# Performance work log

Measured on AMD Instinct MI355X. Metric: run time of the kernel, lower is better.

## Reference

```python
import jax, jax.numpy as jnp
import numpy as np


def setup_inputs() -> dict:
    key = jax.random.key(0)
    k1, k2, k3 = jax.random.split(key, 3)
    N, K, d, d_out = 100000, 32, 64, 64
    x = jax.random.normal(k1, (N, d), dtype=jnp.float32)
    edge_index = jax.random.randint(k2, (N, K), 0, N, dtype=jnp.int64)
    W = jax.random.normal(k3, (2 * d, d_out), dtype=jnp.float32) * (1.0 / np.sqrt(2 * d))
    b = jnp.zeros((d_out,), dtype=jnp.float32)
    return {"x": x, "edge_index": edge_index, "W": W, "b": b}


def reference(x, edge_index, W, b):
    # x: [N, d], edge_index: [N, K] dense neighbor indices
    x_j = x[edge_index]                                  # [N, K, d] gather
    # concat([x_i, x_j - x_i]) then max over K. The x_i half is constant over K,
    # so its max is x itself; max of the diff half computed directly (same math,
    # avoids materializing the [N, K, 2d] concat).
    diff_max = jnp.max(x_j - x[:, None, :], axis=1)      # [N, d]
    h = jnp.concatenate([x, diff_max], axis=-1)          # [N, 2d]
    return h @ W + b                                     # [N, d_out]
```

## Files before the change

### kernel.cpp

```cpp
#include <hip/hip_runtime.h>
#include <hip/hip_bf16.h>
#include <cstdint>


typedef __attribute__((ext_vector_type(8))) short short8;
typedef __attribute__((ext_vector_type(4))) float f4;

#define TILE 16
#define ROWS 168

__device__ __forceinline__ unsigned short f2bf(float f) {
  unsigned int u = __builtin_bit_cast(unsigned int, f);
  u += 0x7fffu + ((u >> 16) & 1u);
  return (unsigned short)(u >> 16);
}
__device__ __forceinline__ unsigned int pack2(float a, float b) {
  return (unsigned int)f2bf(a) | ((unsigned int)f2bf(b) << 16);
}
__device__ __forceinline__ float bflo(unsigned int u) {
  return __builtin_bit_cast(float, u << 16);
}
__device__ __forceinline__ float bfhi(unsigned int u) {
  return __builtin_bit_cast(float, u & 0xffff0000u);
}

__global__ __launch_bounds__(256)
void convert_kernel(const float* __restrict__ x, unsigned int* __restrict__ xbf, int n8) {
  int i = blockIdx.x * 256 + threadIdx.x;
  if (i >= n8) return;
  const f4* p = (const f4*)x + (size_t)i * 2;
  f4 a = p[0], b = p[1];
  uint4 w;
  w.x = pack2(a.x, a.y); w.y = pack2(a.z, a.w);
  w.z = pack2(b.x, b.y); w.w = pack2(b.z, b.w);
  ((uint4*)xbf)[i] = w;
}

__global__ __launch_bounds__(256, 6)
void mrconv2_kernel(const unsigned int* __restrict__ xbf,
                    const int* __restrict__ ei,
                    const float* __restrict__ W,
                    const float* __restrict__ bias,
                    float* __restrict__ out,
                    int n_tiles)
{
  __shared__ __align__(16) unsigned short hs[TILE * ROWS];
  __shared__ __align__(16) int eis[TILE * 32];
  __shared__ __align__(16) float otile[TILE * 64];

  const int tid  = threadIdx.x;
  const int wv   = tid >> 6;
  const int lane = tid & 63;
  const int c = lane & 15;
  const int g = lane >> 4;
  const int t2 = lane >> 5;
  const int h  = (lane >> 3) & 3;
  const int e  = lane & 7;

  const int node0 = blockIdx.x * TILE;

  short8 bfrag[4];
  #pragma unroll
  for (int ks = 0; ks < 4; ++ks) {
    short8 v;
    #pragma unroll
    for (int j = 0; j < 8; ++j)
      v[j] = (short)f2bf(W[(ks * 32 + g * 8 + j) * 64 + wv * 16 + c]);
    bfrag[ks] = v;
  }

  *(int2*)&eis[tid * 2] = *(const int2*)(ei + (size_t)node0 * 32 + tid * 2);
  __syncthreads();

  const float NEG = -3.4e38f;
  #pragma unroll
  for (int tt = 0; tt < 2; ++tt) {
    const int t = wv * 4 + tt * 2 + t2;
    const uint4 xr = *(const uint4*)(xbf + (size_t)(node0 + t) * 32 + e * 4);
    const float xi0 = bflo(xr.x), xi1 = bfhi(xr.x);
    const float xi2 = bflo(xr.y), xi3 = bfhi(xr.y);
    const float xi4 = bflo(xr.z), xi5 = bfhi(xr.z);
    const float xi6 = bflo(xr.w), xi7 = bfhi(xr.w);
    float m0 = NEG, m1 = NEG, m2 = NEG, m3 = NEG;
    float m4 = NEG, m5 = NEG, m6 = NEG, m7 = NEG;
    #pragma unroll
    for (int it = 0; it < 8; ++it) {
      const int j = eis[t * 32 + it * 4 + h];
      const uint4 r = *(const uint4*)(xbf + (size_t)j * 32 + e * 4);
      m0 = fmaxf(m0, bflo(r.x) - xi0);
      m1 = fmaxf(m1, bfhi(r.x) - xi1);
      m2 = fmaxf(m2, bflo(r.y) - xi2);
      m3 = fmaxf(m3, bfhi(r.y) - xi3);
      m4 = fmaxf(m4, bflo(r.z) - xi4);
      m5 = fmaxf(m5, bfhi(r.z) - xi5);
      m6 = fmaxf(m6, bflo(r.w) - xi6);
      m7 = fmaxf(m7, bfhi(r.w) - xi7);
    }
    m0 = fmaxf(m0, __shfl_xor(m0, 8));  m1 = fmaxf(m1, __shfl_xor(m1, 8));
    m2 = fmaxf(m2, __shfl_xor(m2, 8));  m3 = fmaxf(m3, __shfl_xor(m3, 8));
    m4 = fmaxf(m4, __shfl_xor(m4, 8));  m5 = fmaxf(m5, __shfl_xor(m5, 8));
    m6 = fmaxf(m6, __shfl_xor(m6, 8));  m7 = fmaxf(m7, __shfl_xor(m7, 8));
    m0 = fmaxf(m0, __shfl_xor(m0, 16)); m1 = fmaxf(m1, __shfl_xor(m1, 16));
    m2 = fmaxf(m2, __shfl_xor(m2, 16)); m3 = fmaxf(m3, __shfl_xor(m3, 16));
    m4 = fmaxf(m4, __shfl_xor(m4, 16)); m5 = fmaxf(m5, __shfl_xor(m5, 16));
    m6 = fmaxf(m6, __shfl_xor(m6, 16)); m7 = fmaxf(m7, __shfl_xor(m7, 16));

    if (h == 1) {
      *(uint4*)(hs + t * ROWS + e * 8) = xr;
    } else if (h == 0) {
      uint4 w;
      w.x = pack2(m0, m1); w.y = pack2(m2, m3);
      w.z = pack2(m4, m5); w.w = pack2(m6, m7);
      *(uint4*)(hs + t * ROWS + 64 + e * 8) = w;
    }
  }
  __syncthreads();

  f4 acc = {0.f, 0.f, 0.f, 0.f};
  #pragma unroll
  for (int ks = 0; ks < 4; ++ks) {
    short8 a = *(const short8*)(hs + c * ROWS + ks * 32 + g * 8);
    acc = __builtin_amdgcn_mfma_f32_16x16x32_bf16(a, bfrag[ks], acc, 0, 0, 0);
  }

  const float bb = bias[wv * 16 + c];
  #pragma unroll
  for (int j = 0; j < 4; ++j)
    otile[(g * 4 + j) * 64 + wv * 16 + c] = acc[j] + bb;
  __syncthreads();
  *(f4*)(out + (size_t)node0 * 64 + tid * 4) = *(const f4*)&otile[tid * 4];
}

#define FWPB 4
#define FROWS 160
__global__ __launch_bounds__(256, 4)
void mrconv_fp32_kernel(const float* __restrict__ x,
                        const int* __restrict__ ei,
                        const float* __restrict__ W,
                        const float* __restrict__ bias,
                        float* __restrict__ out,
                        int n_tiles)
{
  __shared__ __align__(16) unsigned short hsf[FWPB][TILE * FROWS];
  const int wave = threadIdx.x >> 6;
  const int lane = threadIdx.x & 63;
  const int c = lane & 15;
  const int g = lane >> 4;

  short8 bfrag[4][4];
  #pragma unroll
  for (int ks = 0; ks < 4; ++ks) {
    #pragma unroll
    for (int nt = 0; nt < 4; ++nt) {
      short8 v;
      #pragma unroll
      for (int j = 0; j < 8; ++j) {
        int k = ks * 32 + g * 8 + j;
        v[j] = (short)f2bf(W[k * 64 + nt * 16 + c]);
      }
      bfrag[ks][nt] = v;
    }
  }

  const int tile = blockIdx.x * FWPB + wave;
  if (tile >= n_tiles) return;
  const int node0 = tile * TILE;
  unsigned short* hrow = &hsf[wave][0];

  #pragma unroll 2
  for (int t = 0; t < TILE; ++t) {
    const int n = node0 + t;
    const f4 xi = *(const f4*)(x + (size_t)n * 64 + 4 * c);
    f4 m = { -3.4e38f, -3.4e38f, -3.4e38f, -3.4e38f };
    #pragma unroll
    for (int it = 0; it < 8; ++it) {
      const int j = ei[(size_t)n * 32 + it * 4 + g];
      const f4 xj = *(const f4*)(x + (size_t)j * 64 + 4 * c);
      m.x = fmaxf(m.x, xj.x - xi.x);
      m.y = fmaxf(m.y, xj.y - xi.y);
      m.z = fmaxf(m.z, xj.z - xi.z);
      m.w = fmaxf(m.w, xj.w - xi.w);
    }
    m.x = fmaxf(m.x, __shfl_xor(m.x, 16));
    m.y = fmaxf(m.y, __shfl_xor(m.y, 16));
    m.z = fmaxf(m.z, __shfl_xor(m.z, 16));
    m.w = fmaxf(m.w, __shfl_xor(m.w, 16));
    m.x = fmaxf(m.x, __shfl_xor(m.x, 32));
    m.y = fmaxf(m.y, __shfl_xor(m.y, 32));
    m.z = fmaxf(m.z, __shfl_xor(m.z, 32));
    m.w = fmaxf(m.w, __shfl_xor(m.w, 32));
    if (g == 0) {
      ushort4 p;
      p.x = f2bf(xi.x); p.y = f2bf(xi.y); p.z = f2bf(xi.z); p.w = f2bf(xi.w);
      *(ushort4*)(hrow + t * FROWS + 4 * c) = p;
    } else if (g == 1) {
      ushort4 p;
      p.x = f2bf(m.x); p.y = f2bf(m.y); p.z = f2bf(m.z); p.w = f2bf(m.w);
      *(ushort4*)(hrow + t * FROWS + 64 + 4 * c) = p;
    }
  }
  __asm__ volatile("s_waitcnt lgkmcnt(0)" ::: "memory");

  f4 acc[4] = {{0.f,0.f,0.f,0.f},{0.f,0.f,0.f,0.f},{0.f,0.f,0.f,0.f},{0.f,0.f,0.f,0.f}};
  #pragma unroll
  for (int ks = 0; ks < 4; ++ks) {
    short8 a = *(const short8*)(hrow + c * FROWS + ks * 32 + g * 8);
    #pragma unroll
    for (int nt = 0; nt < 4; ++nt)
      acc[nt] = __builtin_amdgcn_mfma_f32_16x16x32_bf16(a, bfrag[ks][nt], acc[nt], 0, 0, 0);
  }
  const int rbase = node0 + g * 4;
  #pragma unroll
  for (int nt = 0; nt < 4; ++nt) {
    const float bb = bias[nt * 16 + c];
    #pragma unroll
    for (int j = 0; j < 4; ++j)
      out[(size_t)(rbase + j) * 64 + nt * 16 + c] = acc[nt][j] + bb;
  }
}

extern "C" void kernel_launch(void* const* d_in, const int* in_sizes, int n_in,
                              void* d_out, int out_size, void* d_ws, size_t ws_size,
                              hipStream_t stream) {
  const float* x  = (const float*)d_in[0];
  const int*   ei = (const int*)d_in[1];
  const float* W  = (const float*)d_in[2];
  const float* b  = (const float*)d_in[3];
  float* out = (float*)d_out;

  const int N = in_sizes[0] / 64;
  const int n_tiles = N / TILE;

  const size_t need = (size_t)N * 64 * 2;
  if (ws_size >= need) {
    unsigned int* xbf = (unsigned int*)d_ws;
    const int n8 = N * 64 / 8;
    hipLaunchKernelGGL(convert_kernel, dim3((n8 + 255) / 256), dim3(256), 0, stream,
                       x, xbf, n8);
    hipLaunchKernelGGL(mrconv2_kernel, dim3(n_tiles), dim3(256), 0, stream,
                       xbf, ei, W, b, out, n_tiles);
  } else {
    const int blocks = (n_tiles + FWPB - 1) / FWPB;
    hipLaunchKernelGGL(mrconv_fp32_kernel, dim3(blocks), dim3(256), 0, stream,
                       x, ei, W, b, out, n_tiles);
  }
}
```

Before: 135.7 us.

## Prepack bf16 W fragments once, hoist x_i subtraction out of neighbor max

New measurement: 130.6 us. 1.04x faster.

```diff
diff --git a/kernel.cpp b/kernel.cpp
--- a/kernel.cpp
+++ b/kernel.cpp
@@ -25,21 +25,37 @@
 }
 
 __global__ __launch_bounds__(256)
-void convert_kernel(const float* __restrict__ x, unsigned int* __restrict__ xbf, int n8) {
-  int i = blockIdx.x * 256 + threadIdx.x;
-  if (i >= n8) return;
-  const f4* p = (const f4*)x + (size_t)i * 2;
-  f4 a = p[0], b = p[1];
-  uint4 w;
-  w.x = pack2(a.x, a.y); w.y = pack2(a.z, a.w);
-  w.z = pack2(b.x, b.y); w.w = pack2(b.z, b.w);
-  ((uint4*)xbf)[i] = w;
+void convert_kernel(const float* __restrict__ x, unsigned int* __restrict__ xbf,
+                    const float* __restrict__ W, unsigned short* __restrict__ wf,
+                    int n8, int nxb) {
+  if ((int)blockIdx.x < nxb) {
+    int i = blockIdx.x * 256 + threadIdx.x;
+    if (i >= n8) return;
+    const f4* p = (const f4*)x + (size_t)i * 2;
+    f4 a = p[0], b = p[1];
+    uint4 w;
+    w.x = pack2(a.x, a.y); w.y = pack2(a.z, a.w);
+    w.z = pack2(b.x, b.y); w.w = pack2(b.z, b.w);
+    ((uint4*)xbf)[i] = w;
+  } else {
+    #pragma unroll
+    for (int q = 0; q < 4; ++q) {
+      int idx = threadIdx.x * 4 + q;
+      int wv = idx >> 8, ks = (idx >> 6) & 3, l = idx & 63;
+      int c = l & 15, g = l >> 4;
+      short8 v;
+      #pragma unroll
+      for (int j = 0; j < 8; ++j)
+        v[j] = (short)f2bf(W[(ks * 32 + g * 8 + j) * 64 + wv * 16 + c]);
+      *(short8*)(wf + (size_t)idx * 8) = v;
+    }
+  }
 }
 
 __global__ __launch_bounds__(256, 6)
-void mrconv2_kernel(const unsigned int* __restrict__ xbf,
+void mrconv3_kernel(const unsigned int* __restrict__ xbf,
+                    const unsigned short* __restrict__ wf,
                     const int* __restrict__ ei,
-                    const float* __restrict__ W,
                     const float* __restrict__ bias,
                     float* __restrict__ out,
                     int n_tiles)
@@ -53,66 +69,54 @@
   const int lane = tid & 63;
   const int c = lane & 15;
   const int g = lane >> 4;
-  const int t2 = lane >> 5;
-  const int h  = (lane >> 3) & 3;
+  const int t2 = lane >> 4;
+  const int h  = (lane >> 3) & 1;
   const int e  = lane & 7;
 
   const int node0 = blockIdx.x * TILE;
+  const int t = wv * 4 + t2;
 
   short8 bfrag[4];
   #pragma unroll
-  for (int ks = 0; ks < 4; ++ks) {
-    short8 v;
-    #pragma unroll
-    for (int j = 0; j < 8; ++j)
-      v[j] = (short)f2bf(W[(ks * 32 + g * 8 + j) * 64 + wv * 16 + c]);
-    bfrag[ks] = v;
-  }
+  for (int ks = 0; ks < 4; ++ks)
+    bfrag[ks] = *(const short8*)(wf + (size_t)((wv * 4 + ks) * 64 + lane) * 8);
 
   *(int2*)&eis[tid * 2] = *(const int2*)(ei + (size_t)node0 * 32 + tid * 2);
   __syncthreads();
 
   const float NEG = -3.4e38f;
-  #pragma unroll
-  for (int tt = 0; tt < 2; ++tt) {
-    const int t = wv * 4 + tt * 2 + t2;
-    const uint4 xr = *(const uint4*)(xbf + (size_t)(node0 + t) * 32 + e * 4);
-    const float xi0 = bflo(xr.x), xi1 = bfhi(xr.x);
-    const float xi2 = bflo(xr.y), xi3 = bfhi(xr.y);
-    const float xi4 = bflo(xr.z), xi5 = bfhi(xr.z);
-    const float xi6 = bflo(xr.w), xi7 = bfhi(xr.w);
-    float m0 = NEG, m1 = NEG, m2 = NEG, m3 = NEG;
-    float m4 = NEG, m5 = NEG, m6 = NEG, m7 = NEG;
-    #pragma unroll
-    for (int it = 0; it < 8; ++it) {
-      const int j = eis[t * 32 + it * 4 + h];
-      const uint4 r = *(const uint4*)(xbf + (size_t)j * 32 + e * 4);
-      m0 = fmaxf(m0, bflo(r.x) - xi0);
-      m1 = fmaxf(m1, bfhi(r.x) - xi1);
-      m2 = fmaxf(m2, bflo(r.y) - xi2);
-      m3 = fmaxf(m3, bfhi(r.y) - xi3);
-      m4 = fmaxf(m4, bflo(r.z) - xi4);
-      m5 = fmaxf(m5, bfhi(r.z) - xi5);
-      m6 = fmaxf(m6, bflo(r.w) - xi6);
-      m7 = fmaxf(m7, bfhi(r.w) - xi7);
-    }
-    m0 = fmaxf(m0, __shfl_xor(m0, 8));  m1 = fmaxf(m1, __shfl_xor(m1, 8));
-    m2 = fmaxf(m2, __shfl_xor(m2, 8));  m3 = fmaxf(m3, __shfl_xor(m3, 8));
-    m4 = fmaxf(m4, __shfl_xor(m4, 8));  m5 = fmaxf(m5, __shfl_xor(m5, 8));
-    m6 = fmaxf(m6, __shfl_xor(m6, 8));  m7 = fmaxf(m7, __shfl_xor(m7, 8));
-    m0 = fmaxf(m0, __shfl_xor(m0, 16)); m1 = fmaxf(m1, __shfl_xor(m1, 16));
-    m2 = fmaxf(m2, __shfl_xor(m2, 16)); m3 = fmaxf(m3, __shfl_xor(m3, 16));
-    m4 = fmaxf(m4, __shfl_xor(m4, 16)); m5 = fmaxf(m5, __shfl_xor(m5, 16));
-    m6 = fmaxf(m6, __shfl_xor(m6, 16)); m7 = fmaxf(m7, __shfl_xor(m7, 16));
-
-    if (h == 1) {
-      *(uint4*)(hs + t * ROWS + e * 8) = xr;
-    } else if (h == 0) {
-      uint4 w;
-      w.x = pack2(m0, m1); w.y = pack2(m2, m3);
-      w.z = pack2(m4, m5); w.w = pack2(m6, m7);
-      *(uint4*)(hs + t * ROWS + 64 + e * 8) = w;
-    }
+  const uint4 xr = *(const uint4*)(xbf + (size_t)(node0 + t) * 32 + e * 4);
+  float l0 = NEG, h0 = NEG, l1 = NEG, h1 = NEG;
+  float l2 = NEG, h2 = NEG, l3 = NEG, h3 = NEG;
+  #pragma unroll
+  for (int it = 0; it < 16; it += 2) {
+    const int ja = eis[t * 32 + it * 2 + h];
+    const int jb = eis[t * 32 + it * 2 + 2 + h];
+    const uint4 ra = *(const uint4*)(xbf + (size_t)ja * 32 + e * 4);
+    const uint4 rb = *(const uint4*)(xbf + (size_t)jb * 32 + e * 4);
+    l0 = fmaxf(l0, fmaxf(bflo(ra.x), bflo(rb.x)));
+    h0 = fmaxf(h0, fmaxf(bfhi(ra.x), bfhi(rb.x)));
+    l1 = fmaxf(l1, fmaxf(bflo(ra.y), bflo(rb.y)));
+    h1 = fmaxf(h1, fmaxf(bfhi(ra.y), bfhi(rb.y)));
+    l2 = fmaxf(l2, fmaxf(bflo(ra.z), bflo(rb.z)));
+    h2 = fmaxf(h2, fmaxf(bfhi(ra.z), bfhi(rb.z)));
+    l3 = fmaxf(l3, fmaxf(bflo(ra.w), bflo(rb.w)));
+    h3 = fmaxf(h3, fmaxf(bfhi(ra.w), bfhi(rb.w)));
+  }
+  l0 = fmaxf(l0, __shfl_xor(l0, 8));  h0 = fmaxf(h0, __shfl_xor(h0, 8));
+  l1 = fmaxf(l1, __shfl_xor(l1, 8));  h1 = fmaxf(h1, __shfl_xor(h1, 8));
+  l2 = fmaxf(l2, __shfl_xor(l2, 8));  h2 = fmaxf(h2, __shfl_xor(h2, 8));
+  l3 = fmaxf(l3, __shfl_xor(l3, 8));  h3 = fmaxf(h3, __shfl_xor(h3, 8));
+
+  if (h == 0) {
+    uint4 w;
+    w.x = pack2(l0 - bflo(xr.x), h0 - bfhi(xr.x));
+    w.y = pack2(l1 - bflo(xr.y), h1 - bfhi(xr.y));
+    w.z = pack2(l2 - bflo(xr.z), h2 - bfhi(xr.z));
+    w.w = pack2(l3 - bflo(xr.w), h3 - bfhi(xr.w));
+    *(uint4*)(hs + t * ROWS + 64 + e * 8) = w;
+  } else {
+    *(uint4*)(hs + t * ROWS + e * 8) = xr;
   }
   __syncthreads();
 
@@ -231,14 +235,17 @@
   const int N = in_sizes[0] / 64;
   const int n_tiles = N / TILE;
 
-  const size_t need = (size_t)N * 64 * 2;
-  if (ws_size >= need) {
-    unsigned int* xbf = (unsigned int*)d_ws;
-    const int n8 = N * 64 / 8;
-    hipLaunchKernelGGL(convert_kernel, dim3((n8 + 255) / 256), dim3(256), 0, stream,
-                       x, xbf, n8);
-    hipLaunchKernelGGL(mrconv2_kernel, dim3(n_tiles), dim3(256), 0, stream,
-                       xbf, ei, W, b, out, n_tiles);
+  const size_t xbf_bytes = (size_t)N * 64 * 2;
+  const size_t wf_bytes  = 1024 * 16;
+  if (ws_size >= xbf_bytes + wf_bytes) {
+    unsigned int*   xbf = (unsigned int*)d_ws;
+    unsigned short* wf  = (unsigned short*)((char*)d_ws + xbf_bytes);
+    const int n8  = N * 64 / 8;
+    const int nxb = (n8 + 255) / 256;
+    hipLaunchKernelGGL(convert_kernel, dim3(nxb + 1), dim3(256), 0, stream,
+                       x, xbf, W, wf, n8, nxb);
+    hipLaunchKernelGGL(mrconv3_kernel, dim3(n_tiles), dim3(256), 0, stream,
+                       xbf, wf, ei, b, out, n_tiles);
   } else {
     const int blocks = (n_tiles + FWPB - 1) / FWPB;
     hipLaunchKernelGGL(mrconv_fp32_kernel, dim3(blocks), dim3(256), 0, stream,
```
